# Kernel optimization log

Hardware: AMD Instinct MI355X
Metric: run time of the kernel (lower is better)

The kernel has to match this reference:

```python
import jax, jax.numpy as jnp
import numpy as np


def setup_inputs() -> dict:
    key = jax.random.key(0)
    k1, k2 = jax.random.split(key)
    B, S, D = 8, 2048, 1024
    x = jax.random.normal(k1, (B, S, D), dtype=jnp.float32)
    # xavier_uniform init for [D, D]
    limit = float(np.sqrt(6.0 / (D + D)))
    att_weight = jax.random.uniform(k2, (D, D), dtype=jnp.float32, minval=-limit, maxval=limit)
    bias = jnp.zeros((D,), dtype=jnp.float32)
    return {"x": x, "att_weight": att_weight, "bias": bias}


def reference(x, att_weight, bias):
    # Q = x @ W; K = V = x
    q = jnp.einsum("bsd,de->bse", x, att_weight)
    scale = 1.0 / jnp.sqrt(jnp.asarray(x.shape[-1], dtype=jnp.float32))
    scores = jnp.einsum("bqd,bkd->bqk", q, x) * scale  # [B,S,S]
    attn = jax.nn.softmax(scores, axis=-1)
    out = jnp.einsum("bqk,bkd->bqd", attn, x)
    return out + bias[None, None, :]
```

## Files before the change

### kernel.cpp

```cpp
#include <hip/hip_runtime.h>

typedef unsigned short u16;
typedef unsigned int u32;
typedef __attribute__((ext_vector_type(8))) short short8;
typedef __attribute__((ext_vector_type(4))) float floatx4;

__device__ __forceinline__ u16 f2bf(float f) {
  u32 u = __float_as_uint(f);
  u32 r = u + 0x7fffu + ((u >> 16) & 1u);
  return (u16)(r >> 16);
}

__device__ __forceinline__ void gload_lds16(const u16* g, u16* l) {
  __builtin_amdgcn_global_load_lds(
      (const __attribute__((address_space(1))) u32*)g,
      (__attribute__((address_space(3))) u32*)l, 16, 0, 0);
}

__global__ __launch_bounds__(256)
void cast_tr(const float* __restrict__ in, u16* __restrict__ cast_out,
             u16* __restrict__ tr_out, int rows, int cols, float scale,
             long bstride)
{
  __shared__ u16 tileT[64][66];
  const int b = blockIdx.z;
  in += (long)b * bstride;
  if (cast_out) cast_out += (long)b * bstride;
  tr_out += (long)b * bstride;
  const int r0 = blockIdx.y * 64, c0 = blockIdx.x * 64;
  const int tid = threadIdx.x;

  {
    const int i0 = tid >> 4;
    const int c4 = (tid & 15) * 4;
    #pragma unroll
    for (int rr = 0; rr < 4; ++rr) {
      const int r = i0 + 16 * rr;
      const float4 v = *(const float4*)&in[(long)(r0 + r) * cols + c0 + c4];
      ushort4 h;
      h.x = f2bf(v.x * scale); h.y = f2bf(v.y * scale);
      h.z = f2bf(v.z * scale); h.w = f2bf(v.w * scale);
      if (cast_out)
        *(ushort4*)&cast_out[(long)(r0 + r) * cols + c0 + c4] = h;
      tileT[c4 + 0][r] = h.x;
      tileT[c4 + 1][r] = h.y;
      tileT[c4 + 2][r] = h.z;
      tileT[c4 + 3][r] = h.w;
    }
  }
  __syncthreads();

  {
    const int cb = tid >> 5;
    const int rh = tid & 31;
    #pragma unroll
    for (int m = 0; m < 8; ++m) {
      const int c = cb * 8 + m;
      const u32 pair = *(const u32*)&tileT[c][rh * 2];
      *(u32*)&tr_out[(long)(c0 + c) * rows + r0 + rh * 2] = pair;
    }
  }
}

#define BK 64

template<int MODE, int MI, int NJ>
__global__ __launch_bounds__(256, 3)
void gemm_nt(const u16* __restrict__ A, const u16* __restrict__ Bt,
             void* __restrict__ Cout, const float* __restrict__ bias,
             float* __restrict__ rsum,
             int M, int N, int K, int lda, int ldb, int ldc,
             long sA, long sB, long sC, float escale)
{
  constexpr int BM = MI * 32;
  constexpr int BN = NJ * 32;
  __shared__ __align__(16) u16 As[BM * BK];
  __shared__ __align__(16) u16 Bs[BN * BK];

  const int bz = blockIdx.z;
  A  += (long)bz * sA;
  Bt += (long)bz * sB;

  const int tid  = threadIdx.x;
  const int wave = tid >> 6;
  const int lane = tid & 63;

  const int nbx = gridDim.x, nby = gridDim.y;
  const int pid  = blockIdx.y * nbx + blockIdx.x;
  const int band = 8 * nbx;
  const int gid  = pid / band;
  const int fm   = gid * 8;
  const int gsz  = min(nby - fm, 8);
  const int pm   = fm + (pid % band) % gsz;
  const int pn   = (pid % band) / gsz;
  const int tileM = pm * BM;
  const int tileN = pn * BN;

  const int srow = lane >> 3;
  const int sj   = lane & 7;
  const int sjj  = sj ^ srow;

  const int wm = (wave >> 1) * (MI * 16);
  const int wn = (wave & 1) * (NJ * 16);
  const int lc = lane & 15;
  const int lq = lane >> 4;

  floatx4 acc[MI][NJ];
  #pragma unroll
  for (int i = 0; i < MI; ++i)
    #pragma unroll
    for (int j = 0; j < NJ; ++j)
      acc[i][j] = (floatx4){0.f, 0.f, 0.f, 0.f};

  for (int k0 = 0; k0 < K; k0 += BK) {
    #pragma unroll
    for (int s = 0; s < MI; ++s) {
      const int rb = (wave * MI + s) * 8;
      gload_lds16(A + (long)(tileM + rb + srow) * lda + k0 + sjj * 8,
                  &As[rb * BK]);
    }
    #pragma unroll
    for (int s = 0; s < NJ; ++s) {
      const int rb = (wave * NJ + s) * 8;
      gload_lds16(Bt + (long)(tileN + rb + srow) * ldb + k0 + sjj * 8,
                  &Bs[rb * BK]);
    }
    __syncthreads();

    #pragma unroll
    for (int kk = 0; kk < BK; kk += 32) {
      const int jcb = (kk >> 3) + lq;
      short8 af[MI], bf[NJ];
      #pragma unroll
      for (int i = 0; i < MI; ++i) {
        const int m = wm + i * 16 + lc;
        af[i] = *(const short8*)&As[m * BK + ((jcb ^ (m & 7)) << 3)];
      }
      #pragma unroll
      for (int j = 0; j < NJ; ++j) {
        const int n = wn + j * 16 + lc;
        bf[j] = *(const short8*)&Bs[n * BK + ((jcb ^ (n & 7)) << 3)];
      }
      #pragma unroll
      for (int i = 0; i < MI; ++i)
        #pragma unroll
        for (int j = 0; j < NJ; ++j)
          acc[i][j] = __builtin_amdgcn_mfma_f32_16x16x32_bf16(
                          af[i], bf[j], acc[i][j], 0, 0, 0);
    }
    __syncthreads();
  }

  if (MODE == 0) {
    u16* C = (u16*)Cout + (long)bz * sC;
    #pragma unroll
    for (int i = 0; i < MI; ++i) {
      const int rb = tileM + wm + i * 16 + lq * 4;
      #pragma unroll
      for (int j = 0; j < NJ; ++j) {
        const int col = tileN + wn + j * 16 + lc;
        #pragma unroll
        for (int r = 0; r < 4; ++r)
          C[(long)(rb + r) * ldc + col] = f2bf(acc[i][j][r]);
      }
    }
  } else if (MODE == 1) {
    u16* C = (u16*)Cout + (long)bz * sC;
    float* rs = rsum + (long)bz * M;
    #pragma unroll
    for (int i = 0; i < MI; ++i) {
      const int rb = tileM + wm + i * 16 + lq * 4;
      float rpart[4] = {0.f, 0.f, 0.f, 0.f};
      #pragma unroll
      for (int j = 0; j < NJ; ++j) {
        const int col = tileN + wn + j * 16 + lc;
        #pragma unroll
        for (int r = 0; r < 4; ++r) {
          float e = __expf(acc[i][j][r] * escale);
          C[(long)(rb + r) * ldc + col] = f2bf(e);
          rpart[r] += e;
        }
      }
      #pragma unroll
      for (int r = 0; r < 4; ++r) {
        float s = rpart[r];
        s += __shfl_xor(s, 1, 64);
        s += __shfl_xor(s, 2, 64);
        s += __shfl_xor(s, 4, 64);
        s += __shfl_xor(s, 8, 64);
        if (lc == 0) atomicAdd(&rs[rb + r], s);
      }
    }
  } else {
    float* C = (float*)Cout + (long)bz * sC;
    const float* rs = rsum + (long)bz * M;
    #pragma unroll
    for (int i = 0; i < MI; ++i) {
      const int rb = tileM + wm + i * 16 + lq * 4;
      float inv[4];
      #pragma unroll
      for (int r = 0; r < 4; ++r) inv[r] = 1.0f / rs[rb + r];
      #pragma unroll
      for (int j = 0; j < NJ; ++j) {
        const int col = tileN + wn + j * 16 + lc;
        const float bv = bias[col];
        #pragma unroll
        for (int r = 0; r < 4; ++r)
          C[(long)(rb + r) * ldc + col] = acc[i][j][r] * inv[r] + bv;
      }
    }
  }
}

extern "C" void kernel_launch(void* const* d_in, const int* in_sizes, int n_in,
                              void* d_out, int out_size, void* d_ws, size_t ws_size,
                              hipStream_t stream) {
  const float* x    = (const float*)d_in[0];
  const float* W    = (const float*)d_in[1];
  const float* bias = (const float*)d_in[2];
  float* out        = (float*)d_out;
  (void)in_sizes; (void)n_in; (void)out_size; (void)ws_size;

  const int B = 8, S = 2048, D = 1024;
  const long BSD = (long)B * S * D;

  u16* Xb  = (u16*)d_ws;
  u16* XbT = Xb  + BSD;
  u16* Qb  = XbT + BSD;
  u16* Wt  = Qb  + BSD;
  u16* Sc  = Wt  + (long)D * D;
  float* rsum = (float*)(Sc + (long)B * S * S);

  dim3 blk(256);

  hipMemsetAsync(rsum, 0, (size_t)B * S * sizeof(float), stream);

  cast_tr<<<dim3(D/64, S/64, B), blk, 0, stream>>>(x, Xb, XbT, S, D, 1.0f, (long)S*D);
  cast_tr<<<dim3(D/64, D/64, 1), blk, 0, stream>>>(W, nullptr, Wt, D, D, 0.03125f, 0);

  gemm_nt<0, 4, 4><<<dim3(D/128, (B*S)/128, 1), blk, 0, stream>>>(
      Xb, Wt, Qb, nullptr, nullptr, B*S, D, D, D, D, D, 0, 0, 0, 1.0f);

  gemm_nt<1, 4, 4><<<dim3(S/128, S/128, B), blk, 0, stream>>>(
      Qb, Xb, Sc, nullptr, rsum, S, S, D, D, D, S,
      (long)S*D, (long)S*D, (long)S*S, 1.0f);

  gemm_nt<2, 4, 4><<<dim3(D/128, S/128, B), blk, 0, stream>>>(
      Sc, XbT, out, bias, rsum, S, D, S, S, S, D,
      (long)S*S, (long)D*S, (long)S*D, 1.0f);
}
```

Before: 321.1 us.

## Use 256x256 double-buffered GEMM tiles with interleaved prefetch and MFMA priority

Replaces the 128x128 single-buffered GEMM with a 512-thread kernel that computes 256x256 tiles. It double-buffers LDS, issues the next k-tile's global-to-LDS loads between quadrant compute phases, and raises wave priority around MFMA bursts. The aim is to hide load latency and raise arithmetic intensity per LDS byte. In exchange it uses 128KB of LDS and more registers per block, and the grid has fewer blocks, which can cost occupancy and tail balance.

New measurement: 317.1 us. Within noise of the previous version (-1.3%).

```diff
diff --git a/kernel.cpp b/kernel.cpp
--- a/kernel.cpp
+++ b/kernel.cpp
@@ -16,6 +16,18 @@
       (const __attribute__((address_space(1))) u32*)g,
       (__attribute__((address_space(3))) u32*)l, 16, 0, 0);
 }
+
+__device__ __forceinline__ void block_bar() {
+  __builtin_amdgcn_sched_barrier(0);
+  __builtin_amdgcn_s_barrier();
+  __builtin_amdgcn_sched_barrier(0);
+}
+
+#define WAITVM0() do {                                   \
+    __builtin_amdgcn_sched_barrier(0);                   \
+    asm volatile("s_waitcnt vmcnt(0)" ::: "memory");     \
+    __builtin_amdgcn_sched_barrier(0);                   \
+  } while (0)
 
 __global__ __launch_bounds__(256)
 void cast_tr(const float* __restrict__ in, u16* __restrict__ cast_out,
@@ -49,7 +61,6 @@
     }
   }
   __syncthreads();
-
   {
     const int cb = tid >> 5;
     const int rh = tid & 31;
@@ -62,20 +73,15 @@
   }
 }
 
-#define BK 64
-
-template<int MODE, int MI, int NJ>
-__global__ __launch_bounds__(256, 3)
-void gemm_nt(const u16* __restrict__ A, const u16* __restrict__ Bt,
+template<int MODE>
+__global__ __launch_bounds__(512, 2)
+void gemm256(const u16* __restrict__ A, const u16* __restrict__ Bt,
              void* __restrict__ Cout, const float* __restrict__ bias,
              float* __restrict__ rsum,
              int M, int N, int K, int lda, int ldb, int ldc,
              long sA, long sB, long sC, float escale)
 {
-  constexpr int BM = MI * 32;
-  constexpr int BN = NJ * 32;
-  __shared__ __align__(16) u16 As[BM * BK];
-  __shared__ __align__(16) u16 Bs[BN * BK];
+  __shared__ __align__(16) u16 lds[2][2][256 * 64];
 
   const int bz = blockIdx.z;
   A  += (long)bz * sA;
@@ -93,71 +99,153 @@
   const int gsz  = min(nby - fm, 8);
   const int pm   = fm + (pid % band) % gsz;
   const int pn   = (pid % band) / gsz;
-  const int tileM = pm * BM;
-  const int tileN = pn * BN;
-
+  const int tileM = pm * 256;
+  const int tileN = pn * 256;
+
+  const int w32  = wave * 32;
   const int srow = lane >> 3;
-  const int sj   = lane & 7;
-  const int sjj  = sj ^ srow;
-
-  const int wm = (wave >> 1) * (MI * 16);
-  const int wn = (wave & 1) * (NJ * 16);
+  const int sjj  = (lane & 7) ^ srow;
+  const u16* pA = A  + (long)(tileM + w32 + srow) * lda + sjj * 8;
+  const u16* pB = Bt + (long)(tileN + w32 + srow) * ldb + sjj * 8;
+
+#define STAGE_A(DST, K0)                                                  \
+    _Pragma("unroll")                                                     \
+    for (int s2 = 0; s2 < 4; ++s2)                                        \
+      gload_lds16(pA + (long)(s2 * 8) * lda + (K0),                       \
+                  &(DST)[(w32 + s2 * 8) * 64]);
+#define STAGE_B(DST, K0)                                                  \
+    _Pragma("unroll")                                                     \
+    for (int s2 = 0; s2 < 4; ++s2)                                        \
+      gload_lds16(pB + (long)(s2 * 8) * ldb + (K0),                       \
+                  &(DST)[(w32 + s2 * 8) * 64]);
+
+  const int wm = (wave >> 2) * 128;
+  const int wn = (wave & 3) * 64;
   const int lc = lane & 15;
   const int lq = lane >> 4;
-
-  floatx4 acc[MI][NJ];
+  const int xr = lc & 7;
+
+  const int ab0 = (wm + lc) * 64 + (((0 + lq) ^ xr) << 3);
+  const int ab1 = (wm + lc) * 64 + (((4 + lq) ^ xr) << 3);
+  const int bb0 = (wn + lc) * 64 + (((0 + lq) ^ xr) << 3);
+  const int bb1 = (wn + lc) * 64 + (((4 + lq) ^ xr) << 3);
+
+  floatx4 acc[8][4];
   #pragma unroll
-  for (int i = 0; i < MI; ++i)
-    #pragma unroll
-    for (int j = 0; j < NJ; ++j)
+  for (int i = 0; i < 8; ++i)
+    #pragma unroll
+    for (int j = 0; j < 4; ++j)
       acc[i][j] = (floatx4){0.f, 0.f, 0.f, 0.f};
 
-  for (int k0 = 0; k0 < K; k0 += BK) {
-    #pragma unroll
-    for (int s = 0; s < MI; ++s) {
-      const int rb = (wave * MI + s) * 8;
-      gload_lds16(A + (long)(tileM + rb + srow) * lda + k0 + sjj * 8,
-                  &As[rb * BK]);
-    }
-    #pragma unroll
-    for (int s = 0; s < NJ; ++s) {
-      const int rb = (wave * NJ + s) * 8;
-      gload_lds16(Bt + (long)(tileN + rb + srow) * ldb + k0 + sjj * 8,
-                  &Bs[rb * BK]);
-    }
-    __syncthreads();
-
-    #pragma unroll
-    for (int kk = 0; kk < BK; kk += 32) {
-      const int jcb = (kk >> 3) + lq;
-      short8 af[MI], bf[NJ];
-      #pragma unroll
-      for (int i = 0; i < MI; ++i) {
-        const int m = wm + i * 16 + lc;
-        af[i] = *(const short8*)&As[m * BK + ((jcb ^ (m & 7)) << 3)];
-      }
-      #pragma unroll
-      for (int j = 0; j < NJ; ++j) {
-        const int n = wn + j * 16 + lc;
-        bf[j] = *(const short8*)&Bs[n * BK + ((jcb ^ (n & 7)) << 3)];
-      }
-      #pragma unroll
-      for (int i = 0; i < MI; ++i)
-        #pragma unroll
-        for (int j = 0; j < NJ; ++j)
+  const int NT = K >> 6;
+
+  STAGE_A(lds[0][0], 0)
+  STAGE_B(lds[0][1], 0)
+  WAITVM0();
+  block_bar();
+
+  short8 a[4][2], b[2][2];
+
+  for (int t = 0; t < NT; ++t) {
+    const int s = t & 1;
+    const u16* As = &lds[s][0][0];
+    const u16* Bs = &lds[s][1][0];
+    u16* nA = &lds[s ^ 1][0][0];
+    u16* nB = &lds[s ^ 1][1][0];
+    const long nk = (long)(t + 1) << 6;
+    const bool pf = (t + 1) < NT;
+
+    #pragma unroll
+    for (int i = 0; i < 4; ++i) {
+      a[i][0] = *(const short8*)&As[ab0 + i * 1024];
+      a[i][1] = *(const short8*)&As[ab1 + i * 1024];
+    }
+    #pragma unroll
+    for (int j = 0; j < 2; ++j) {
+      b[j][0] = *(const short8*)&Bs[bb0 + j * 1024];
+      b[j][1] = *(const short8*)&Bs[bb1 + j * 1024];
+    }
+    if (pf) { STAGE_A(nA, nk) }
+    block_bar();
+    __builtin_amdgcn_s_setprio(1);
+    #pragma unroll
+    for (int h = 0; h < 2; ++h)
+      #pragma unroll
+      for (int i = 0; i < 4; ++i)
+        #pragma unroll
+        for (int j = 0; j < 2; ++j)
           acc[i][j] = __builtin_amdgcn_mfma_f32_16x16x32_bf16(
-                          af[i], bf[j], acc[i][j], 0, 0, 0);
-    }
-    __syncthreads();
+                          a[i][h], b[j][h], acc[i][j], 0, 0, 0);
+    __builtin_amdgcn_s_setprio(0);
+    block_bar();
+
+    #pragma unroll
+    for (int j = 0; j < 2; ++j) {
+      b[j][0] = *(const short8*)&Bs[bb0 + (j + 2) * 1024];
+      b[j][1] = *(const short8*)&Bs[bb1 + (j + 2) * 1024];
+    }
+    if (pf) { STAGE_B(nB, nk) }
+    block_bar();
+    __builtin_amdgcn_s_setprio(1);
+    #pragma unroll
+    for (int h = 0; h < 2; ++h)
+      #pragma unroll
+      for (int i = 0; i < 4; ++i)
+        #pragma unroll
+        for (int j = 0; j < 2; ++j)
+          acc[i][j + 2] = __builtin_amdgcn_mfma_f32_16x16x32_bf16(
+                          a[i][h], b[j][h], acc[i][j + 2], 0, 0, 0);
+    __builtin_amdgcn_s_setprio(0);
+    block_bar();
+
+    #pragma unroll
+    for (int i = 0; i < 4; ++i) {
+      a[i][0] = *(const short8*)&As[ab0 + (i + 4) * 1024];
+      a[i][1] = *(const short8*)&As[ab1 + (i + 4) * 1024];
+    }
+    block_bar();
+    __builtin_amdgcn_s_setprio(1);
+    #pragma unroll
+    for (int h = 0; h < 2; ++h)
+      #pragma unroll
+      for (int i = 0; i < 4; ++i)
+        #pragma unroll
+        for (int j = 0; j < 2; ++j)
+          acc[i + 4][j + 2] = __builtin_amdgcn_mfma_f32_16x16x32_bf16(
+                          a[i][h], b[j][h], acc[i + 4][j + 2], 0, 0, 0);
+    __builtin_amdgcn_s_setprio(0);
+    block_bar();
+
+    #pragma unroll
+    for (int j = 0; j < 2; ++j) {
+      b[j][0] = *(const short8*)&Bs[bb0 + j * 1024];
+      b[j][1] = *(const short8*)&Bs[bb1 + j * 1024];
+    }
+    block_bar();
+    __builtin_amdgcn_s_setprio(1);
+    #pragma unroll
+    for (int h = 0; h < 2; ++h)
+      #pragma unroll
+      for (int i = 0; i < 4; ++i)
+        #pragma unroll
+        for (int j = 0; j < 2; ++j)
+          acc[i + 4][j] = __builtin_amdgcn_mfma_f32_16x16x32_bf16(
+                          a[i][h], b[j][h], acc[i + 4][j], 0, 0, 0);
+    __builtin_amdgcn_s_setprio(0);
+    WAITVM0();
+    block_bar();
   }
+
+#undef STAGE_A
+#undef STAGE_B
 
   if (MODE == 0) {
     u16* C = (u16*)Cout + (long)bz * sC;
     #pragma unroll
-    for (int i = 0; i < MI; ++i) {
+    for (int i = 0; i < 8; ++i) {
       const int rb = tileM + wm + i * 16 + lq * 4;
       #pragma unroll
-      for (int j = 0; j < NJ; ++j) {
+      for (int j = 0; j < 4; ++j) {
         const int col = tileN + wn + j * 16 + lc;
         #pragma unroll
         for (int r = 0; r < 4; ++r)
@@ -168,11 +256,11 @@
     u16* C = (u16*)Cout + (long)bz * sC;
     float* rs = rsum + (long)bz * M;
     #pragma unroll
-    for (int i = 0; i < MI; ++i) {
+    for (int i = 0; i < 8; ++i) {
       const int rb = tileM + wm + i * 16 + lq * 4;
       float rpart[4] = {0.f, 0.f, 0.f, 0.f};
       #pragma unroll
-      for (int j = 0; j < NJ; ++j) {
+      for (int j = 0; j < 4; ++j) {
         const int col = tileN + wn + j * 16 + lc;
         #pragma unroll
         for (int r = 0; r < 4; ++r) {
@@ -183,25 +271,25 @@
       }
       #pragma unroll
       for (int r = 0; r < 4; ++r) {
-        float s = rpart[r];
-        s += __shfl_xor(s, 1, 64);
-        s += __shfl_xor(s, 2, 64);
-        s += __shfl_xor(s, 4, 64);
-        s += __shfl_xor(s, 8, 64);
-        if (lc == 0) atomicAdd(&rs[rb + r], s);
+        float v = rpart[r];
+        v += __shfl_xor(v, 1, 64);
+        v += __shfl_xor(v, 2, 64);
+        v += __shfl_xor(v, 4, 64);
+        v += __shfl_xor(v, 8, 64);
+        if (lc == 0) atomicAdd(&rs[rb + r], v);
       }
     }
   } else {
     float* C = (float*)Cout + (long)bz * sC;
     const float* rs = rsum + (long)bz * M;
     #pragma unroll
-    for (int i = 0; i < MI; ++i) {
+    for (int i = 0; i < 8; ++i) {
       const int rb = tileM + wm + i * 16 + lq * 4;
       float inv[4];
       #pragma unroll
       for (int r = 0; r < 4; ++r) inv[r] = 1.0f / rs[rb + r];
       #pragma unroll
-      for (int j = 0; j < NJ; ++j) {
+      for (int j = 0; j < 4; ++j) {
         const int col = tileN + wn + j * 16 + lc;
         const float bv = bias[col];
         #pragma unroll
@@ -232,20 +320,21 @@
   float* rsum = (float*)(Sc + (long)B * S * S);
 
   dim3 blk(256);
+  dim3 blk2(512);
 
   hipMemsetAsync(rsum, 0, (size_t)B * S * sizeof(float), stream);
 
   cast_tr<<<dim3(D/64, S/64, B), blk, 0, stream>>>(x, Xb, XbT, S, D, 1.0f, (long)S*D);
   cast_tr<<<dim3(D/64, D/64, 1), blk, 0, stream>>>(W, nullptr, Wt, D, D, 0.03125f, 0);
 
-  gemm_nt<0, 4, 4><<<dim3(D/128, (B*S)/128, 1), blk, 0, stream>>>(
+  gemm256<0><<<dim3(D/256, (B*S)/256, 1), blk2, 0, stream>>>(
       Xb, Wt, Qb, nullptr, nullptr, B*S, D, D, D, D, D, 0, 0, 0, 1.0f);
 
-  gemm_nt<1, 4, 4><<<dim3(S/128, S/128, B), blk, 0, stream>>>(
+  gemm256<1><<<dim3(S/256, S/256, B), blk2, 0, stream>>>(
       Qb, Xb, Sc, nullptr, rsum, S, S, D, D, D, S,
       (long)S*D, (long)S*D, (long)S*S, 1.0f);
 
-  gemm_nt<2, 4, 4><<<dim3(D/128, S/128, B), blk, 0, stream>>>(
+  gemm256<2><<<dim3(D/256, S/256, B), blk2, 0, stream>>>(
       Sc, XbT, out, bias, rsum, S, D, S, S, S, D,
       (long)S*S, (long)D*S, (long)S*D, 1.0f);
 }
```

## Replace 128x128 GEMM with 256x256 double-buffered 8-wave ping-pong pipelined kernel

Applied to the files above, without the earlier changes.

Replaces the single-buffered 128x128 bf16 MFMA GEMM with a 256x256 tile kernel using 512 threads (8 waves). The kernel double-buffers K-tiles in LDS, prefetches two tiles ahead with direct global-to-LDS loads and explicit vmcnt waits, and interleaves quadrant MFMA groups with barriers and setprio. The aim is more data reuse per loaded byte and overlap of global loads with MFMA work, where the old kernel stalled on a sync around each tile. The cost is 128KB of LDS per block, more accumulator registers, and fewer blocks in the grid, which may lower occupancy and leave the Q projection GEMM with a small grid.

After: 328.7 us. 1.02x slower.

```diff
diff --git a/kernel.cpp b/kernel.cpp
--- a/kernel.cpp
+++ b/kernel.cpp
@@ -16,6 +16,14 @@
       (const __attribute__((address_space(1))) u32*)g,
       (__attribute__((address_space(3))) u32*)l, 16, 0, 0);
 }
+
+__device__ __forceinline__ void bar() { __builtin_amdgcn_s_barrier(); }
+
+#define WAITVM(N) do {                                        \
+    __builtin_amdgcn_sched_barrier(0);                        \
+    asm volatile("s_waitcnt vmcnt(" #N ")" ::: "memory");     \
+    __builtin_amdgcn_sched_barrier(0);                        \
+  } while (0)
 
 __global__ __launch_bounds__(256)
 void cast_tr(const float* __restrict__ in, u16* __restrict__ cast_out,
@@ -49,7 +57,6 @@
     }
   }
   __syncthreads();
-
   {
     const int cb = tid >> 5;
     const int rh = tid & 31;
@@ -62,20 +69,16 @@
   }
 }
 
-#define BK 64
-
-template<int MODE, int MI, int NJ>
-__global__ __launch_bounds__(256, 3)
-void gemm_nt(const u16* __restrict__ A, const u16* __restrict__ Bt,
+template<int MODE>
+__global__ __launch_bounds__(512, 2)
+void gemm256(const u16* __restrict__ A, const u16* __restrict__ Bt,
              void* __restrict__ Cout, const float* __restrict__ bias,
              float* __restrict__ rsum,
              int M, int N, int K, int lda, int ldb, int ldc,
              long sA, long sB, long sC, float escale)
 {
-  constexpr int BM = MI * 32;
-  constexpr int BN = NJ * 32;
-  __shared__ __align__(16) u16 As[BM * BK];
-  __shared__ __align__(16) u16 Bs[BN * BK];
+  __shared__ __align__(16) u16 ldsA[4 * 8192];
+  __shared__ __align__(16) u16 ldsB[4 * 8192];
 
   const int bz = blockIdx.z;
   A  += (long)bz * sA;
@@ -93,122 +96,194 @@
   const int gsz  = min(nby - fm, 8);
   const int pm   = fm + (pid % band) % gsz;
   const int pn   = (pid % band) / gsz;
-  const int tileM = pm * BM;
-  const int tileN = pn * BN;
+  const int tileM = pm * 256;
+  const int tileN = pn * 256;
 
   const int srow = lane >> 3;
-  const int sj   = lane & 7;
-  const int sjj  = sj ^ srow;
-
-  const int wm = (wave >> 1) * (MI * 16);
-  const int wn = (wave & 1) * (NJ * 16);
+  const int sjj  = (lane & 7) ^ srow;
+  const u16* pA = A  + (long)(tileM + wave * 16 + srow) * lda + sjj * 8;
+  const u16* pB = Bt + (long)(tileN + wave * 16 + srow) * ldb + sjj * 8;
+  const int wso = wave * 1024;
+
+#define STG_A(kt, h) do {                                                  \
+    u16* d = ldsA + ((((kt) & 1) * 2 + (h)) * 8192) + wso;                 \
+    const u16* g = pA + (long)((h) * 128) * lda + (long)(kt) * 64;         \
+    gload_lds16(g, d); gload_lds16(g + (long)8 * lda, d + 512);            \
+  } while (0)
+#define STG_B(kt, h) do {                                                  \
+    u16* d = ldsB + ((((kt) & 1) * 2 + (h)) * 8192) + wso;                 \
+    const u16* g = pB + (long)((h) * 128) * ldb + (long)(kt) * 64;         \
+    gload_lds16(g, d); gload_lds16(g + (long)8 * ldb, d + 512);            \
+  } while (0)
+
+  const int wv2 = wave >> 2;
+  const int wv4 = wave & 3;
   const int lc = lane & 15;
   const int lq = lane >> 4;
-
-  floatx4 acc[MI][NJ];
+  const int x8 = lc & 7;
+
+  const int aoff0 = (wv2 * 64 + lc) * 64 + (((0 + lq) ^ x8) << 3);
+  const int aoff1 = (wv2 * 64 + lc) * 64 + (((4 + lq) ^ x8) << 3);
+  const int boff0 = (wv4 * 32 + lc) * 64 + (((0 + lq) ^ x8) << 3);
+  const int boff1 = (wv4 * 32 + lc) * 64 + (((4 + lq) ^ x8) << 3);
+
+  floatx4 accq[2][2][4][2];
   #pragma unroll
-  for (int i = 0; i < MI; ++i)
-    #pragma unroll
-    for (int j = 0; j < NJ; ++j)
-      acc[i][j] = (floatx4){0.f, 0.f, 0.f, 0.f};
-
-  for (int k0 = 0; k0 < K; k0 += BK) {
-    #pragma unroll
-    for (int s = 0; s < MI; ++s) {
-      const int rb = (wave * MI + s) * 8;
-      gload_lds16(A + (long)(tileM + rb + srow) * lda + k0 + sjj * 8,
-                  &As[rb * BK]);
-    }
-    #pragma unroll
-    for (int s = 0; s < NJ; ++s) {
-      const int rb = (wave * NJ + s) * 8;
-      gload_lds16(Bt + (long)(tileN + rb + srow) * ldb + k0 + sjj * 8,
-                  &Bs[rb * BK]);
-    }
-    __syncthreads();
-
-    #pragma unroll
-    for (int kk = 0; kk < BK; kk += 32) {
-      const int jcb = (kk >> 3) + lq;
-      short8 af[MI], bf[NJ];
+  for (int qm = 0; qm < 2; ++qm)
+    #pragma unroll
+    for (int qn = 0; qn < 2; ++qn)
       #pragma unroll
-      for (int i = 0; i < MI; ++i) {
-        const int m = wm + i * 16 + lc;
-        af[i] = *(const short8*)&As[m * BK + ((jcb ^ (m & 7)) << 3)];
-      }
-      #pragma unroll
-      for (int j = 0; j < NJ; ++j) {
-        const int n = wn + j * 16 + lc;
-        bf[j] = *(const short8*)&Bs[n * BK + ((jcb ^ (n & 7)) << 3)];
-      }
-      #pragma unroll
-      for (int i = 0; i < MI; ++i)
-        #pragma unroll
-        for (int j = 0; j < NJ; ++j)
-          acc[i][j] = __builtin_amdgcn_mfma_f32_16x16x32_bf16(
-                          af[i], bf[j], acc[i][j], 0, 0, 0);
-    }
-    __syncthreads();
+      for (int mi = 0; mi < 4; ++mi)
+        #pragma unroll
+        for (int nj = 0; nj < 2; ++nj)
+          accq[qm][qn][mi][nj] = (floatx4){0.f, 0.f, 0.f, 0.f};
+
+  const int NT = K >> 6;
+
+  STG_A(0, 0); STG_A(0, 1); STG_B(0, 0); STG_B(0, 1);
+  STG_A(1, 0); STG_A(1, 1); STG_B(1, 0); STG_B(1, 1);
+  WAITVM(8);
+  bar();
+
+#define MFMA_Q(QM, QN, BF)                                                 \
+    __builtin_amdgcn_s_setprio(1);                                        \
+    _Pragma("unroll")                                                     \
+    for (int kh = 0; kh < 2; ++kh)                                        \
+      _Pragma("unroll")                                                   \
+      for (int mi = 0; mi < 4; ++mi)                                      \
+        _Pragma("unroll")                                                 \
+        for (int nj = 0; nj < 2; ++nj)                                    \
+          accq[QM][QN][mi][nj] = __builtin_amdgcn_mfma_f32_16x16x32_bf16( \
+              af[mi][kh], BF[nj][kh], accq[QM][QN][mi][nj], 0, 0, 0);     \
+    __builtin_amdgcn_s_setprio(0);
+
+  short8 af[4][2], bq0[2][2], bq1[2][2];
+
+  for (int t = 0; t < NT; ++t) {
+    const int s2 = (t & 1) * 2;
+    const u16* As0 = ldsA + (s2 + 0) * 8192;
+    const u16* As1 = ldsA + (s2 + 1) * 8192;
+    const u16* Bs0 = ldsB + (s2 + 0) * 8192;
+    const u16* Bs1 = ldsB + (s2 + 1) * 8192;
+    const bool stg = (t + 2) < NT;
+
+    #pragma unroll
+    for (int mi = 0; mi < 4; ++mi) {
+      af[mi][0] = *(const short8*)&As0[aoff0 + mi * 1024];
+      af[mi][1] = *(const short8*)&As0[aoff1 + mi * 1024];
+    }
+    #pragma unroll
+    for (int nj = 0; nj < 2; ++nj) {
+      bq0[nj][0] = *(const short8*)&Bs0[boff0 + nj * 1024];
+      bq0[nj][1] = *(const short8*)&Bs0[boff1 + nj * 1024];
+    }
+    bar();
+    MFMA_Q(0, 0, bq0);
+    bar();
+
+    #pragma unroll
+    for (int nj = 0; nj < 2; ++nj) {
+      bq1[nj][0] = *(const short8*)&Bs1[boff0 + nj * 1024];
+      bq1[nj][1] = *(const short8*)&Bs1[boff1 + nj * 1024];
+    }
+    if (stg) { STG_A(t + 2, 0); STG_B(t + 2, 0); }
+    bar();
+    MFMA_Q(0, 1, bq1);
+    bar();
+
+    #pragma unroll
+    for (int mi = 0; mi < 4; ++mi) {
+      af[mi][0] = *(const short8*)&As1[aoff0 + mi * 1024];
+      af[mi][1] = *(const short8*)&As1[aoff1 + mi * 1024];
+    }
+    if (stg) { STG_B(t + 2, 1); }
+    bar();
+    MFMA_Q(1, 1, bq1);
+    bar();
+
+    if (stg) { STG_A(t + 2, 1); }
+    bar();
+    MFMA_Q(1, 0, bq0);
+    if (t < NT - 1) {
+      if (stg) { WAITVM(8); } else { WAITVM(0); }
+      bar();
+    }
   }
+
+#undef STG_A
+#undef STG_B
+#undef MFMA_Q
 
   if (MODE == 0) {
     u16* C = (u16*)Cout + (long)bz * sC;
     #pragma unroll
-    for (int i = 0; i < MI; ++i) {
-      const int rb = tileM + wm + i * 16 + lq * 4;
+    for (int qm = 0; qm < 2; ++qm)
       #pragma unroll
-      for (int j = 0; j < NJ; ++j) {
-        const int col = tileN + wn + j * 16 + lc;
-        #pragma unroll
-        for (int r = 0; r < 4; ++r)
-          C[(long)(rb + r) * ldc + col] = f2bf(acc[i][j][r]);
+      for (int mi = 0; mi < 4; ++mi) {
+        const int rb = tileM + qm * 128 + wv2 * 64 + mi * 16 + lq * 4;
+        #pragma unroll
+        for (int qn = 0; qn < 2; ++qn)
+          #pragma unroll
+          for (int nj = 0; nj < 2; ++nj) {
+            const int col = tileN + qn * 128 + wv4 * 32 + nj * 16 + lc;
+            #pragma unroll
+            for (int r = 0; r < 4; ++r)
+              C[(long)(rb + r) * ldc + col] = f2bf(accq[qm][qn][mi][nj][r]);
+          }
       }
-    }
   } else if (MODE == 1) {
     u16* C = (u16*)Cout + (long)bz * sC;
     float* rs = rsum + (long)bz * M;
     #pragma unroll
-    for (int i = 0; i < MI; ++i) {
-      const int rb = tileM + wm + i * 16 + lq * 4;
-      float rpart[4] = {0.f, 0.f, 0.f, 0.f};
+    for (int qm = 0; qm < 2; ++qm)
       #pragma unroll
-      for (int j = 0; j < NJ; ++j) {
-        const int col = tileN + wn + j * 16 + lc;
+      for (int mi = 0; mi < 4; ++mi) {
+        const int rb = tileM + qm * 128 + wv2 * 64 + mi * 16 + lq * 4;
+        float rpart[4] = {0.f, 0.f, 0.f, 0.f};
+        #pragma unroll
+        for (int qn = 0; qn < 2; ++qn)
+          #pragma unroll
+          for (int nj = 0; nj < 2; ++nj) {
+            const int col = tileN + qn * 128 + wv4 * 32 + nj * 16 + lc;
+            #pragma unroll
+            for (int r = 0; r < 4; ++r) {
+              float e = __expf(accq[qm][qn][mi][nj][r] * escale);
+              C[(long)(rb + r) * ldc + col] = f2bf(e);
+              rpart[r] += e;
+            }
+          }
         #pragma unroll
         for (int r = 0; r < 4; ++r) {
-          float e = __expf(acc[i][j][r] * escale);
-          C[(long)(rb + r) * ldc + col] = f2bf(e);
-          rpart[r] += e;
+          float v = rpart[r];
+          v += __shfl_xor(v, 1, 64);
+          v += __shfl_xor(v, 2, 64);
+          v += __shfl_xor(v, 4, 64);
+          v += __shfl_xor(v, 8, 64);
+          if (lc == 0) atomicAdd(&rs[rb + r], v);
         }
       }
-      #pragma unroll
-      for (int r = 0; r < 4; ++r) {
-        float s = rpart[r];
-        s += __shfl_xor(s, 1, 64);
-        s += __shfl_xor(s, 2, 64);
-        s += __shfl_xor(s, 4, 64);
-        s += __shfl_xor(s, 8, 64);
-        if (lc == 0) atomicAdd(&rs[rb + r], s);
-      }
-    }
   } else {
     float* C = (float*)Cout + (long)bz * sC;
     const float* rs = rsum + (long)bz * M;
     #pragma unroll
-    for (int i = 0; i < MI; ++i) {
-      const int rb = tileM + wm + i * 16 + lq * 4;
-      float inv[4];
+    for (int qm = 0; qm < 2; ++qm)
       #pragma unroll
-      for (int r = 0; r < 4; ++r) inv[r] = 1.0f / rs[rb + r];
-      #pragma unroll
-      for (int j = 0; j < NJ; ++j) {
-        const int col = tileN + wn + j * 16 + lc;
-        const float bv = bias[col];
-        #pragma unroll
-        for (int r = 0; r < 4; ++r)
-          C[(long)(rb + r) * ldc + col] = acc[i][j][r] * inv[r] + bv;
+      for (int mi = 0; mi < 4; ++mi) {
+        const int rb = tileM + qm * 128 + wv2 * 64 + mi * 16 + lq * 4;
+        float inv[4];
+        #pragma unroll
+        for (int r = 0; r < 4; ++r) inv[r] = 1.0f / rs[rb + r];
+        #pragma unroll
+        for (int qn = 0; qn < 2; ++qn)
+          #pragma unroll
+          for (int nj = 0; nj < 2; ++nj) {
+            const int col = tileN + qn * 128 + wv4 * 32 + nj * 16 + lc;
+            const float bv = bias[col];
+            #pragma unroll
+            for (int r = 0; r < 4; ++r)
+              C[(long)(rb + r) * ldc + col] = accq[qm][qn][mi][nj][r] * inv[r] + bv;
+          }
       }
-    }
   }
 }
 
@@ -232,20 +307,21 @@
   float* rsum = (float*)(Sc + (long)B * S * S);
 
   dim3 blk(256);
+  dim3 blk2(512);
 
   hipMemsetAsync(rsum, 0, (size_t)B * S * sizeof(float), stream);
 
   cast_tr<<<dim3(D/64, S/64, B), blk, 0, stream>>>(x, Xb, XbT, S, D, 1.0f, (long)S*D);
   cast_tr<<<dim3(D/64, D/64, 1), blk, 0, stream>>>(W, nullptr, Wt, D, D, 0.03125f, 0);
 
-  gemm_nt<0, 4, 4><<<dim3(D/128, (B*S)/128, 1), blk, 0, stream>>>(
+  gemm256<0><<<dim3(D/256, (B*S)/256, 1), blk2, 0, stream>>>(
       Xb, Wt, Qb, nullptr, nullptr, B*S, D, D, D, D, D, 0, 0, 0, 1.0f);
 
-  gemm_nt<1, 4, 4><<<dim3(S/128, S/128, B), blk, 0, stream>>>(
+  gemm256<1><<<dim3(S/256, S/256, B), blk2, 0, stream>>>(
       Qb, Xb, Sc, nullptr, rsum, S, S, D, D, D, S,
       (long)S*D, (long)S*D, (long)S*S, 1.0f);
 
-  gemm_nt<2, 4, 4><<<dim3(D/128, S/128, B), blk, 0, stream>>>(
+  gemm256<2><<<dim3(D/256, S/256, B), blk2, 0, stream>>>(
       Sc, XbT, out, bias, rsum, S, D, S, S, S, D,
       (long)S*S, (long)D*S, (long)S*D, 1.0f);
 }
```
